# Performance work log

Measured on AMD Instinct MI355X. Metric: run time of the kernel, lower is better.

## Reference

```python
import jax, jax.numpy as jnp
import numpy as np

N_NODES = 50000
N_EDGES = 800000
H_DIM = 128
HIDDEN = 256


def _glorot(key, shape):
    fan_in, fan_out = shape[1], shape[0]
    lim = np.sqrt(6.0 / (fan_in + fan_out)).astype(np.float32)
    return jax.random.uniform(key, shape, jnp.float32, -lim, lim)


def setup_inputs() -> dict:
    key = jax.random.key(0)
    ks = jax.random.split(key, 12)
    h = jax.random.normal(ks[0], (N_NODES, H_DIM), jnp.float32)
    coord_diff = jax.random.normal(ks[1], (N_EDGES, 3), jnp.float32)
    row = jax.random.randint(ks[2], (N_EDGES,), 0, N_NODES, jnp.int64)
    col = jax.random.randint(ks[3], (N_EDGES,), 0, N_NODES, jnp.int64)
    # edge MLP: Linear(2*H+1 -> HIDDEN), SiLU, Linear(HIDDEN -> HIDDEN), SiLU
    We1 = _glorot(ks[4], (HIDDEN, 2 * H_DIM + 1))
    be1 = jnp.zeros((HIDDEN,), jnp.float32)
    We2 = _glorot(ks[5], (HIDDEN, HIDDEN))
    be2 = jnp.zeros((HIDDEN,), jnp.float32)
    # node MLP: Linear(HIDDEN + H -> HIDDEN), SiLU, Linear(HIDDEN -> H)
    Wn1 = _glorot(ks[6], (HIDDEN, HIDDEN + H_DIM))
    bn1 = jnp.zeros((HIDDEN,), jnp.float32)
    Wn2 = _glorot(ks[7], (H_DIM, HIDDEN))
    bn2 = jnp.zeros((H_DIM,), jnp.float32)
    return {"h": h, "coord_diff": coord_diff, "row": row, "col": col,
            "We1": We1, "be1": be1, "We2": We2, "be2": be2,
            "Wn1": Wn1, "bn1": bn1, "Wn2": Wn2, "bn2": bn2}


def reference(h, coord_diff, row, col, We1, be1, We2, be2, Wn1, bn1, Wn2, bn2):
    # radial: squared edge length, [E, 1]
    radial = jnp.sum(coord_diff ** 2, axis=1, keepdims=True)
    # edge model: gather endpoints, concat, 2-layer SiLU MLP
    e_in = jnp.concatenate([h[row], h[col], radial], axis=1)  # [E, 2H+1]
    m = jax.nn.silu(e_in @ We1.T + be1)                        # [E, HIDDEN]
    m = jax.nn.silu(m @ We2.T + be2)                           # [E, HIDDEN]
    # node model: scatter-add messages to source node `row`
    agg = jax.ops.segment_sum(m, row, num_segments=h.shape[0])  # [N, HIDDEN]
    n_in = jnp.concatenate([h, agg], axis=1)                    # [N, HIDDEN+H]
    out = jax.nn.silu(n_in @ Wn1.T + bn1) @ Wn2.T + bn2         # [N, H]
    return out
```

## Files before the change

kernel.cpp:

```cpp
#include <hip/hip_runtime.h>
#include <cstdint>
#include <cstddef>

#define E_EDGES 800000
#define N_NODES 50000
#define HDIM 128
#define HID 256
#define ME 64
#define NB 64
#define NTILES 196

typedef __attribute__((ext_vector_type(8))) short short8;
typedef __attribute__((ext_vector_type(4))) float f32x4;
typedef __attribute__((ext_vector_type(2))) float f32x2;
typedef __attribute__((ext_vector_type(4))) unsigned int u32x4;

__device__ __forceinline__ float silu(float y) {
    return y * __builtin_amdgcn_rcpf(1.0f + __expf(-y));
}

__device__ __forceinline__ f32x2 silu2(f32x2 y) {
    f32x2 nn = y * (-1.44269504f);
    f32x2 e;
    e.x = __builtin_amdgcn_exp2f(nn.x);
    e.y = __builtin_amdgcn_exp2f(nn.y);
    f32x2 den = e + 1.0f;
    f32x2 r;
    r.x = __builtin_amdgcn_rcpf(den.x);
    r.y = __builtin_amdgcn_rcpf(den.y);
    return y * r;
}

__device__ __forceinline__ f32x2 unpk(unsigned int d) {
    f32x2 r;
    r.x = __uint_as_float(d << 16);
    r.y = __uint_as_float(d & 0xFFFF0000u);
    return r;
}

__device__ __forceinline__ short f2bfn(float f) {
    __bf16 b = (__bf16)f;
    return __builtin_bit_cast(short, b);
}
__device__ __forceinline__ float bf2f(short s) {
    return __uint_as_float(((unsigned int)(unsigned short)s) << 16);
}

#define PREP_H    6250
#define PREP_AGG  (PREP_H + 12500)
#define PREP_HIST (PREP_AGG + 3125)
#define PREP_WAB  (PREP_HIST + 320)
#define PREP_WRF  (PREP_WAB + 1)
#define PREP_WE2  (PREP_WRF + 288)
#define PREP_WN1  (PREP_WE2 + 416)
#define PREP_WN2  (PREP_WN1 + 144)
__global__ void prep_kernel(const float* __restrict__ h, short* __restrict__ hbf,
                            float* __restrict__ agg,
                            const int* __restrict__ row, int* __restrict__ cnt,
                            const float* __restrict__ We1, const float* __restrict__ be1,
                            short* __restrict__ Wab, float* __restrict__ wrf,
                            const float* __restrict__ We2, const float* __restrict__ be2,
                            short* __restrict__ Wb2,
                            const float* __restrict__ Wn1, const float* __restrict__ bn1,
                            short* __restrict__ Wbn1,
                            const float* __restrict__ Wn2, const float* __restrict__ bn2,
                            short* __restrict__ Wbn2) {
    const int b = blockIdx.x, t = threadIdx.x;
    if (b < PREP_H) {
        int i = b * 256 + t;
        float4 v = ((const float4*)h)[i];
        short4 s;
        s.x = f2bfn(v.x); s.y = f2bfn(v.y); s.z = f2bfn(v.z); s.w = f2bfn(v.w);
        ((short4*)hbf)[i] = s;
    } else if (b < PREP_AGG) {
        int i = (b - PREP_H) * 256 + t;
        ((float4*)agg)[i] = make_float4(0.f, 0.f, 0.f, 0.f);
    } else if (b < PREP_HIST) {
        int e = (b - PREP_AGG) * 256 + t;
        if (e < E_EDGES) atomicAdd(&cnt[row[e]], 1);
    } else if (b < PREP_WAB) {
        int idx = (b - PREP_HIST) * 256 + t;
        int c = idx / 160, k = idx - c * 160;
        short v = 0;
        if (c < 256) {
            if (k < 128)       v = f2bfn(We1[c * 257 + k]);
            else if (k == 128) v = f2bfn(be1[c]);
        } else {
            if (k < 128)       v = f2bfn(We1[(c - 256) * 257 + 128 + k]);
        }
        Wab[idx] = v;
    } else if (b < PREP_WRF) {
        wrf[t] = We1[t * 257 + 256];
    } else if (b < PREP_WE2) {
        int idx = (b - PREP_WRF) * 256 + t;
        int c = idx / 288, k = idx - c * 288;
        short v = 0;
        if (k < 256)       v = f2bfn(We2[c * 256 + k]);
        else if (k == 256) v = f2bfn(be2[c]);
        Wb2[idx] = v;
    } else if (b < PREP_WN1) {
        int idx = (b - PREP_WE2) * 256 + t;
        int c = idx / 416, k = idx - c * 416;
        short v = 0;
        if (k < 384)       v = f2bfn(Wn1[c * 384 + k]);
        else if (k == 384) v = f2bfn(bn1[c]);
        Wbn1[idx] = v;
    } else {
        int idx = (b - PREP_WN1) * 256 + t;
        int c = idx / 288, k = idx - c * 288;
        short v = 0;
        if (k < 256)       v = f2bfn(Wn2[c * 256 + k]);
        else if (k == 256) v = f2bfn(bn2[c]);
        Wbn2[idx] = v;
    }
}

__global__ void scanA_kernel(const int* __restrict__ cnt, int* __restrict__ incl,
                             int* __restrict__ tsum) {
    const int b = blockIdx.x, t = threadIdx.x;
    const int i = b * 256 + t;
    const int lane = t & 63, wv = t >> 6;
    int v = (i < N_NODES) ? cnt[i] : 0;
    int s = v;
#pragma unroll
    for (int off = 1; off < 64; off <<= 1) {
        int u = __shfl_up(s, off, 64);
        if (lane >= off) s += u;
    }
    __shared__ int wsum[4];
    if (lane == 63) wsum[wv] = s;
    __syncthreads();
    int pre = 0;
#pragma unroll
    for (int j = 0; j < 3; ++j) if (wv > j) pre += wsum[j];
    s += pre;
    if (i < N_NODES) incl[i] = s;
    if (t == 255) tsum[b] = s;
}

__global__ void scanB_kernel(const int* __restrict__ tsum, int* __restrict__ toff) {
    const int t = threadIdx.x;
    const int lane = t & 63, wv = t >> 6;
    int v = (t < NTILES) ? tsum[t] : 0;
    int s = v;
#pragma unroll
    for (int off = 1; off < 64; off <<= 1) {
        int u = __shfl_up(s, off, 64);
        if (lane >= off) s += u;
    }
    __shared__ int wsum[4];
    if (lane == 63) wsum[wv] = s;
    __syncthreads();
    int pre = 0;
#pragma unroll
    for (int j = 0; j < 3; ++j) if (wv > j) pre += wsum[j];
    s += pre;
    if (t < NTILES) toff[t] = s - v;
}

__global__ void scanC_kernel(const int* __restrict__ cnt, int* __restrict__ cursor,
                             const int* __restrict__ toff) {
    const int b = blockIdx.x, t = threadIdx.x;
    const int i = b * 256 + t;
    if (i < N_NODES) {
        cursor[i] = cursor[i] - cnt[i] + toff[b];
    }
}

__global__ void fill_kernel(const int* __restrict__ row, int* __restrict__ cursor,
                            int* __restrict__ eidx) {
    int e = blockIdx.x * 256 + threadIdx.x;
    if (e < E_EDGES) {
        int pos = atomicAdd(&cursor[row[e]], 1);
        eidx[pos] = e;
    }
}

__global__ __launch_bounds__(256, 4) void hab_kernel(
    const short* __restrict__ hbf, const short* __restrict__ Wab,
    short* __restrict__ hab)
{
    __shared__ __align__(16) short pool[NB * 256];
    __shared__ __align__(16) short shTh[NB * 32];
    short* shH = pool;
    short* shO = pool;

    const int t = threadIdx.x;
    const int tile = blockIdx.x >> 1;
    const int half = blockIdx.x & 1;
    const int n0 = tile * NB;

    {
        const int n = t >> 2, q = t & 3;
        int gn = n0 + n;
        if (gn >= N_NODES) gn = N_NODES - 1;
        const short8* hp = (const short8*)(hbf + (size_t)gn * HDIM + q * 32);
#pragma unroll
        for (int c = 0; c < 4; ++c) {
            short8 v = hp[c];
            int chunk = q * 4 + c;
            *(short8*)&shH[n * 128 + ((chunk ^ (n & 7)) << 3)] = v;
        }
        short8 z = {0, 0, 0, 0, 0, 0, 0, 0};
        if (q == 0) z[0] = (short)0x3F80;
        *(short8*)&shTh[n * 32 + ((q ^ (n & 3)) << 3)] = z;
    }
    __syncthreads();

    const int l = t & 63, w = t >> 6;
    const int l15 = l & 15, lq = l >> 4;

    f32x4 acc[4][4];
#pragma unroll
    for (int i = 0; i < 4; ++i)
#pragma unroll
        for (int j = 0; j < 4; ++j) acc[i][j] = (f32x4){0.f, 0.f, 0.f, 0.f};

#pragma unroll
    for (int ks = 0; ks < 5; ++ks) {
        short8 a[4], b[4];
#pragma unroll
        for (int et = 0; et < 4; ++et) {
            int r = et * 16 + l15;
            if (ks < 4) {
                int chunk = ks * 4 + lq;
                a[et] = *(const short8*)&shH[r * 128 + ((chunk ^ (r & 7)) << 3)];
            } else {
                a[et] = *(const short8*)&shTh[r * 32 + ((lq ^ (r & 3)) << 3)];
            }
        }
#pragma unroll
        for (int ct = 0; ct < 4; ++ct) {
            int cc = half * 256 + w * 64 + ct * 16 + l15;
            b[ct] = *(const short8*)&Wab[cc * 160 + ks * 32 + lq * 8];
        }
#pragma unroll
        for (int et = 0; et < 4; ++et)
#pragma unroll
            for (int ct = 0; ct < 4; ++ct)
                acc[ct][et] = __builtin_amdgcn_mfma_f32_16x16x32_bf16(
                    b[ct], a[et], acc[ct][et], 0, 0, 0);
    }
    __syncthreads();

    {
#pragma unroll
        for (int ct = 0; ct < 4; ++ct) {
#pragma unroll
            for (int et = 0; et < 4; ++et) {
                int n = et * 16 + l15;
                int chb = w * 64 + ct * 16 + lq * 4;
                short4 s;
                s.x = f2bfn(acc[ct][et][0]);
                s.y = f2bfn(acc[ct][et][1]);
                s.z = f2bfn(acc[ct][et][2]);
                s.w = f2bfn(acc[ct][et][3]);
                int chunk = chb >> 3;
                *(short4*)&shO[n * 256 + ((chunk ^ (n & 7)) << 3) + (chb & 7)] = s;
            }
        }
    }
    __syncthreads();

    {
        const int n = t >> 2, q = t & 3;
        int gn = n0 + n;
        if (gn < N_NODES) {
            short* dst = hab + (size_t)gn * 512 + half * 256;
#pragma unroll
            for (int c = 0; c < 8; ++c) {
                int chunk = c * 4 + q;
                short8 v = *(const short8*)&shO[n * 256 + ((chunk ^ (n & 7)) << 3)];
                *(short8*)&dst[chunk * 8] = v;
            }
        }
    }
}

__global__ __launch_bounds__(256, 4) void edge_kernel(
    const short* __restrict__ hab, const float* __restrict__ coord,
    const int* __restrict__ row, const int* __restrict__ col,
    const int* __restrict__ eidx, const float* __restrict__ wrf,
    const short* __restrict__ Wb2, float* __restrict__ agg)
{
    __shared__ __align__(16) short shPool[ME * 256 + ME * 32];
    __shared__ int sr[ME];
    short* shA = shPool;
    short* shT = shPool + ME * 256;

    const int t = threadIdx.x;
    const int nwg = E_EDGES / ME;
    const int qq = nwg >> 3, rr = nwg & 7;
    const int xcd = blockIdx.x & 7, bi = blockIdx.x >> 3;
    const int wg = (xcd < rr ? xcd * (qq + 1) : rr * (qq + 1) + (xcd - rr) * qq) + bi;
    const int e0 = wg * ME;

    {
        const int e = t >> 2, q = t & 3;
        const int eo = eidx[e0 + e];
        const int rsrc = row[eo];
        const int csrc = col[eo];
        const short8* Ap = (const short8*)(hab + (size_t)rsrc * 512 + q * 64);
        const short8* Bp = (const short8*)(hab + (size_t)csrc * 512 + 256 + q * 64);
        short8 av[8], bv[8];
#pragma unroll
        for (int j = 0; j < 8; ++j) av[j] = Ap[j];
#pragma unroll
        for (int j = 0; j < 8; ++j) bv[j] = Bp[j];
        float cx = coord[3 * eo + 0];
        float cy = coord[3 * eo + 1];
        float cz = coord[3 * eo + 2];
        float radial = cx * cx + cy * cy + cz * cz;
        const f32x2* Wp2 = (const f32x2*)(wrf + q * 64);
#pragma unroll
        for (int j = 0; j < 8; ++j) {
            u32x4 ua = __builtin_bit_cast(u32x4, av[j]);
            u32x4 ub = __builtin_bit_cast(u32x4, bv[j]);
            short8 o;
#pragma unroll
            for (int u = 0; u < 4; ++u) {
                f32x2 af = unpk(ua[u]);
                f32x2 bf = unpk(ub[u]);
                f32x2 y = af + bf;
                y += radial * Wp2[4 * j + u];
                f32x2 s2 = silu2(y);
                o[2 * u]     = f2bfn(s2.x);
                o[2 * u + 1] = f2bfn(s2.y);
            }
            int chunk = q * 8 + j;
            *(short8*)&shA[e * 256 + ((chunk ^ (e & 7)) << 3)] = o;
        }
        short8 z = {0, 0, 0, 0, 0, 0, 0, 0};
        if (q == 0) {
            z[0] = (short)0x3F80;
            sr[e] = rsrc;
        }
        *(short8*)&shT[e * 32 + ((q ^ (e & 3)) << 3)] = z;
    }
    __syncthreads();

    const int l = t & 63, w = t >> 6;
    const int l15 = l & 15, lq = l >> 4;

    f32x4 acc[4][4];
#pragma unroll
    for (int i = 0; i < 4; ++i)
#pragma unroll
        for (int j = 0; j < 4; ++j) acc[i][j] = (f32x4){0.f, 0.f, 0.f, 0.f};
#pragma unroll
    for (int ks = 0; ks < 8; ++ks) {
        short8 a[4], b[4];
#pragma unroll
        for (int et = 0; et < 4; ++et) {
            int r = et * 16 + l15;
            int chunk = ks * 4 + lq;
            a[et] = *(const short8*)&shA[r * 256 + ((chunk ^ (r & 7)) << 3)];
        }
#pragma unroll
        for (int ct = 0; ct < 4; ++ct) {
            int cc = w * 64 + ct * 16 + l15;
            b[ct] = *(const short8*)&Wb2[cc * 288 + ks * 32 + lq * 8];
        }
        __builtin_amdgcn_s_setprio(1);
#pragma unroll
        for (int et = 0; et < 4; ++et)
#pragma unroll
            for (int ct = 0; ct < 4; ++ct)
                acc[et][ct] = __builtin_amdgcn_mfma_f32_16x16x32_bf16(
                    a[et], b[ct], acc[et][ct], 0, 0, 0);
        __builtin_amdgcn_s_setprio(0);
    }
    {
        short8 a[4], b[4];
#pragma unroll
        for (int et = 0; et < 4; ++et) {
            int r = et * 16 + l15;
            a[et] = *(const short8*)&shT[r * 32 + ((lq ^ (r & 3)) << 3)];
        }
#pragma unroll
        for (int ct = 0; ct < 4; ++ct) {
            int cc = w * 64 + ct * 16 + l15;
            b[ct] = *(const short8*)&Wb2[cc * 288 + 256 + lq * 8];
        }
        __builtin_amdgcn_s_setprio(1);
#pragma unroll
        for (int et = 0; et < 4; ++et)
#pragma unroll
            for (int ct = 0; ct < 4; ++ct)
                acc[et][ct] = __builtin_amdgcn_mfma_f32_16x16x32_bf16(
                    a[et], b[ct], acc[et][ct], 0, 0, 0);
        __builtin_amdgcn_s_setprio(0);
    }
    __syncthreads();

    {
#pragma unroll
        for (int ct = 0; ct < 4; ++ct) {
#pragma unroll
            for (int et = 0; et < 4; ++et) {
                int kc = w * 64 + ct * 16 + l15;
                int er0 = et * 16 + lq * 4;
                f32x2 p0 = {acc[et][ct][0], acc[et][ct][1]};
                f32x2 p1 = {acc[et][ct][2], acc[et][ct][3]};
                f32x2 s0 = silu2(p0);
                f32x2 s1 = silu2(p1);
                short4 s;
                s.x = f2bfn(s0.x);
                s.y = f2bfn(s0.y);
                s.z = f2bfn(s1.x);
                s.w = f2bfn(s1.y);
                *(short4*)&shPool[kc * 68 + er0] = s;
            }
        }
    }
    __syncthreads();

    {
        const int cc = t;
        const short* myrow = &shPool[cc * 68];
        float accum = 0.f;
        int cur = __builtin_amdgcn_readfirstlane(sr[0]);
        bool headSeg = true;
        for (int eb = 0; eb < ME; eb += 4) {
            short4 v4 = *(const short4*)&myrow[eb];
            short vj[4] = {v4.x, v4.y, v4.z, v4.w};
#pragma unroll
            for (int j = 0; j < 4; ++j) {
                float v = bf2f(vj[j]);
                int r = __builtin_amdgcn_readfirstlane(sr[eb + j]);
                if (r != cur) {
                    if (headSeg) {
                        atomicAdd(&agg[(size_t)cur * HID + cc], accum);
                        headSeg = false;
                    } else {
                        agg[(size_t)cur * HID + cc] = accum;
                    }
                    accum = v;
                    cur = r;
                } else {
                    accum += v;
                }
            }
        }
        atomicAdd(&agg[(size_t)cur * HID + cc], accum);
    }
}

__global__ __launch_bounds__(256, 3) void node_kernel(
    const short* __restrict__ hbf, const float* __restrict__ agg,
    const short* __restrict__ Wbn1, const short* __restrict__ Wbn2,
    float* __restrict__ out)
{
    __shared__ __align__(16) short pool[NB * 384];
    __shared__ __align__(16) short shTn[NB * 32];
    short* shH  = pool;
    short* shAg = pool + NB * 128;
    short* shM  = pool;

    const int t  = threadIdx.x;
    const int n0 = blockIdx.x * NB;

    {
        const int n = t >> 2, q = t & 3;
        int gn = n0 + n;
        if (gn >= N_NODES) gn = N_NODES - 1;
        const short8* hp = (const short8*)(hbf + (size_t)gn * HDIM + q * 32);
#pragma unroll
        for (int c = 0; c < 4; ++c) {
            short8 v = hp[c];
            int chunk = q * 4 + c;
            int sw = chunk ^ (n & 7);
            *(short8*)&shH[n * 128 + sw * 8] = v;
        }
        const float4* ap = (const float4*)(agg + (size_t)gn * HID + q * 64);
#pragma unroll
        for (int i = 0; i < 8; ++i) {
            float4 u0 = ap[2 * i], u1 = ap[2 * i + 1];
            short8 s;
            s[0] = f2bfn(u0.x); s[1] = f2bfn(u0.y); s[2] = f2bfn(u0.z); s[3] = f2bfn(u0.w);
            s[4] = f2bfn(u1.x); s[5] = f2bfn(u1.y); s[6] = f2bfn(u1.z); s[7] = f2bfn(u1.w);
            int chunk = q * 8 + i;
            int sw2 = chunk ^ (n & 7);
            *(short8*)&shAg[n * 256 + sw2 * 8] = s;
        }
        short8 z = {0, 0, 0, 0, 0, 0, 0, 0};
        if (q == 0) z[0] = (short)0x3F80;
        *(short8*)&shTn[n * 32 + ((q ^ (n & 3)) << 3)] = z;
    }
    __syncthreads();

    const int l = t & 63, w = t >> 6;
    const int l15 = l & 15, lq = l >> 4;

    f32x4 acc[4][4];
#pragma unroll
    for (int i = 0; i < 4; ++i)
#pragma unroll
        for (int j = 0; j < 4; ++j) acc[i][j] = (f32x4){0.f, 0.f, 0.f, 0.f};
#pragma unroll
    for (int ks = 0; ks < 12; ++ks) {
        short8 a[4], b[4];
#pragma unroll
        for (int et = 0; et < 4; ++et) {
            int r = et * 16 + l15;
            if (ks < 4) {
                int chunk = ks * 4 + lq;
                a[et] = *(const short8*)&shH[r * 128 + ((chunk ^ (r & 7)) << 3)];
            } else {
                int chunk = (ks - 4) * 4 + lq;
                a[et] = *(const short8*)&shAg[r * 256 + ((chunk ^ (r & 7)) << 3)];
            }
        }
#pragma unroll
        for (int ct = 0; ct < 4; ++ct) {
            int cc = w * 64 + ct * 16 + l15;
            b[ct] = *(const short8*)&Wbn1[cc * 416 + ks * 32 + lq * 8];
        }
#pragma unroll
        for (int et = 0; et < 4; ++et)
#pragma unroll
            for (int ct = 0; ct < 4; ++ct)
                acc[et][ct] = __builtin_amdgcn_mfma_f32_16x16x32_bf16(
                    a[et], b[ct], acc[et][ct], 0, 0, 0);
    }
    {
        short8 a[4], b[4];
#pragma unroll
        for (int et = 0; et < 4; ++et) {
            int r = et * 16 + l15;
            a[et] = *(const short8*)&shTn[r * 32 + ((lq ^ (r & 3)) << 3)];
        }
#pragma unroll
        for (int ct = 0; ct < 4; ++ct) {
            int cc = w * 64 + ct * 16 + l15;
            b[ct] = *(const short8*)&Wbn1[cc * 416 + 384 + lq * 8];
        }
#pragma unroll
        for (int et = 0; et < 4; ++et)
#pragma unroll
            for (int ct = 0; ct < 4; ++ct)
                acc[et][ct] = __builtin_amdgcn_mfma_f32_16x16x32_bf16(
                    a[et], b[ct], acc[et][ct], 0, 0, 0);
    }
    __syncthreads();

    {
#pragma unroll
        for (int et = 0; et < 4; ++et) {
#pragma unroll
            for (int rp = 0; rp < 2; ++rp) {
                int er0 = et * 16 + lq * 4 + rp * 2;
#pragma unroll
                for (int ct = 0; ct < 4; ++ct) {
                    int kc = w * 64 + ct * 16 + l15;
                    float y0 = silu(acc[et][ct][rp * 2]);
                    float y1 = silu(acc[et][ct][rp * 2 + 1]);
                    int khi = kc >> 3, klo = kc & 7;
                    shM[er0 * 256 + ((khi ^ (er0 & 7)) << 3) + klo] = f2bfn(y0);
                    shM[(er0 + 1) * 256 + ((khi ^ ((er0 + 1) & 7)) << 3) + klo] = f2bfn(y1);
                }
            }
        }
    }
    __syncthreads();

    f32x4 acc2[4][2];
#pragma unroll
    for (int i = 0; i < 4; ++i)
#pragma unroll
        for (int j = 0; j < 2; ++j) acc2[i][j] = (f32x4){0.f, 0.f, 0.f, 0.f};
#pragma unroll
    for (int ks = 0; ks < 8; ++ks) {
        short8 a[4], b2[2];
#pragma unroll
        for (int et = 0; et < 4; ++et) {
            int r = et * 16 + l15;
            int chunk = ks * 4 + lq;
            a[et] = *(const short8*)&shM[r * 256 + ((chunk ^ (r & 7)) << 3)];
        }
#pragma unroll
        for (int ct = 0; ct < 2; ++ct) {
            int cc = w * 32 + ct * 16 + l15;
            b2[ct] = *(const short8*)&Wbn2[cc * 288 + ks * 32 + lq * 8];
        }
#pragma unroll
        for (int et = 0; et < 4; ++et)
#pragma unroll
            for (int ct = 0; ct < 2; ++ct)
                acc2[et][ct] = __builtin_amdgcn_mfma_f32_16x16x32_bf16(
                    a[et], b2[ct], acc2[et][ct], 0, 0, 0);
    }
    {
        short8 a[4], b2[2];
#pragma unroll
        for (int et = 0; et < 4; ++et) {
            int r = et * 16 + l15;
            a[et] = *(const short8*)&shTn[r * 32 + ((lq ^ (r & 3)) << 3)];
        }
#pragma unroll
        for (int ct = 0; ct < 2; ++ct) {
            int cc = w * 32 + ct * 16 + l15;
            b2[ct] = *(const short8*)&Wbn2[cc * 288 + 256 + lq * 8];
        }
#pragma unroll
        for (int et = 0; et < 4; ++et)
#pragma unroll
            for (int ct = 0; ct < 2; ++ct)
                acc2[et][ct] = __builtin_amdgcn_mfma_f32_16x16x32_bf16(
                    a[et], b2[ct], acc2[et][ct], 0, 0, 0);
    }

#pragma unroll
    for (int et = 0; et < 4; ++et) {
#pragma unroll
        for (int ct = 0; ct < 2; ++ct) {
            int cc = w * 32 + ct * 16 + l15;
#pragma unroll
            for (int r4 = 0; r4 < 4; ++r4) {
                int gn = n0 + et * 16 + lq * 4 + r4;
                if (gn < N_NODES)
                    out[(size_t)gn * HDIM + cc] = acc2[et][ct][r4];
            }
        }
    }
}

extern "C" void kernel_launch(void* const* d_in, const int* in_sizes, int n_in,
                              void* d_out, int out_size, void* d_ws, size_t ws_size,
                              hipStream_t stream) {
    const float* h   = (const float*)d_in[0];
    const float* cd  = (const float*)d_in[1];
    const int*   row = (const int*)d_in[2];
    const int*   col = (const int*)d_in[3];
    const float* We1 = (const float*)d_in[4];
    const float* be1 = (const float*)d_in[5];
    const float* We2 = (const float*)d_in[6];
    const float* be2 = (const float*)d_in[7];
    const float* Wn1 = (const float*)d_in[8];
    const float* bn1 = (const float*)d_in[9];
    const float* Wn2 = (const float*)d_in[10];
    const float* bn2 = (const float*)d_in[11];
    float* out = (float*)d_out;

    short* Wab  = (short*)d_ws;
    short* Wb2  = Wab + 512 * 160;
    short* Wbn1 = Wb2 + 256 * 288;
    short* Wbn2 = Wbn1 + 256 * 416;
    float* wrf  = (float*)(Wbn2 + 128 * 288);
    short* hbf  = (short*)(wrf + 256);
    short* hab  = hbf + (size_t)N_NODES * HDIM;
    float* agg  = (float*)(hab + (size_t)N_NODES * 512);
    int*   cnt    = (int*)(agg + (size_t)N_NODES * HID);
    int*   cursor = cnt + N_NODES;
    int*   eidx   = cursor + N_NODES;
    int*   tsum   = eidx + E_EDGES;
    int*   toff   = tsum + 256;

    hipMemsetAsync(cnt, 0, N_NODES * sizeof(int), stream);

    prep_kernel<<<PREP_WN2, 256, 0, stream>>>(h, hbf, agg, row, cnt,
                                              We1, be1, Wab, wrf,
                                              We2, be2, Wb2,
                                              Wn1, bn1, Wbn1, Wn2, bn2, Wbn2);

    hab_kernel<<<((N_NODES + NB - 1) / NB) * 2, 256, 0, stream>>>(hbf, Wab, hab);

    scanA_kernel<<<NTILES, 256, 0, stream>>>(cnt, cursor, tsum);
    scanB_kernel<<<1, 256, 0, stream>>>(tsum, toff);
    scanC_kernel<<<NTILES, 256, 0, stream>>>(cnt, cursor, toff);
    fill_kernel<<<(E_EDGES + 255) / 256, 256, 0, stream>>>(row, cursor, eidx);

    edge_kernel<<<E_EDGES / ME, 256, 0, stream>>>(hab, cd, row, col, eidx, wrf,
                                                  Wb2, agg);
    node_kernel<<<(N_NODES + NB - 1) / NB, 256, 0, stream>>>(hbf, agg, Wbn1, Wbn2, out);
}
```

Before: 474.4 us.

## Sort edges by column bucket then row to improve gather locality

Edges are now counting-sorted by a composite key of (col bucket of 6250 nodes, row) instead of by row alone. Each edge tile then gathers col-endpoint features from a narrow node range, which is meant to improve L2 reuse of the hab gathers. The cost is an 8x larger histogram and scan (400k keys across 1563 tiles, with a multi-element-per-thread top-level scan). Because one row's edges are now split across buckets, segment flushes can no longer use plain stores and every flush becomes an atomicAdd, adding atomic traffic on agg.

```diff
diff --git a/kernel.cpp b/kernel.cpp
--- a/kernel.cpp
+++ b/kernel.cpp
@@ -8,7 +8,9 @@
 #define HID 256
 #define ME 64
 #define NB 64
-#define NTILES 196
+#define NBUK_DIV 6250
+#define NKEYS 400000
+#define NT2 1563
 
 typedef __attribute__((ext_vector_type(8))) short short8;
 typedef __attribute__((ext_vector_type(4))) float f32x4;
@@ -56,7 +58,8 @@
 #define PREP_WN2  (PREP_WN1 + 144)
 __global__ void prep_kernel(const float* __restrict__ h, short* __restrict__ hbf,
                             float* __restrict__ agg,
-                            const int* __restrict__ row, int* __restrict__ cnt,
+                            const int* __restrict__ row, const int* __restrict__ col,
+                            int* __restrict__ cnt,
                             const float* __restrict__ We1, const float* __restrict__ be1,
                             short* __restrict__ Wab, float* __restrict__ wrf,
                             const float* __restrict__ We2, const float* __restrict__ be2,
@@ -77,7 +80,10 @@
         ((float4*)agg)[i] = make_float4(0.f, 0.f, 0.f, 0.f);
     } else if (b < PREP_HIST) {
         int e = (b - PREP_AGG) * 256 + t;
-        if (e < E_EDGES) atomicAdd(&cnt[row[e]], 1);
+        if (e < E_EDGES) {
+            int key = (col[e] / NBUK_DIV) * N_NODES + row[e];
+            atomicAdd(&cnt[key], 1);
+        }
     } else if (b < PREP_WAB) {
         int idx = (b - PREP_HIST) * 256 + t;
         int c = idx / 160, k = idx - c * 160;
@@ -120,7 +126,7 @@
     const int b = blockIdx.x, t = threadIdx.x;
     const int i = b * 256 + t;
     const int lane = t & 63, wv = t >> 6;
-    int v = (i < N_NODES) ? cnt[i] : 0;
+    int v = (i < NKEYS) ? cnt[i] : 0;
     int s = v;
 #pragma unroll
     for (int off = 1; off < 64; off <<= 1) {
@@ -134,15 +140,25 @@
 #pragma unroll
     for (int j = 0; j < 3; ++j) if (wv > j) pre += wsum[j];
     s += pre;
-    if (i < N_NODES) incl[i] = s;
+    if (i < NKEYS) incl[i] = s;
     if (t == 255) tsum[b] = s;
 }
 
 __global__ void scanB_kernel(const int* __restrict__ tsum, int* __restrict__ toff) {
     const int t = threadIdx.x;
     const int lane = t & 63, wv = t >> 6;
-    int v = (t < NTILES) ? tsum[t] : 0;
-    int s = v;
+    int vex[7];
+    int run = 0;
+    const int base = t * 7;
+#pragma unroll
+    for (int k = 0; k < 7; ++k) {
+        int idx = base + k;
+        int x = (idx < NT2) ? tsum[idx] : 0;
+        vex[k] = run;
+        run += x;
+    }
+    int tot = run;
+    int s = tot;
 #pragma unroll
     for (int off = 1; off < 64; off <<= 1) {
         int u = __shfl_up(s, off, 64);
@@ -155,23 +171,29 @@
 #pragma unroll
     for (int j = 0; j < 3; ++j) if (wv > j) pre += wsum[j];
     s += pre;
-    if (t < NTILES) toff[t] = s - v;
+    int excl = s - tot;
+#pragma unroll
+    for (int k = 0; k < 7; ++k) {
+        int idx = base + k;
+        if (idx < NT2) toff[idx] = excl + vex[k];
+    }
 }
 
 __global__ void scanC_kernel(const int* __restrict__ cnt, int* __restrict__ cursor,
                              const int* __restrict__ toff) {
     const int b = blockIdx.x, t = threadIdx.x;
     const int i = b * 256 + t;
-    if (i < N_NODES) {
+    if (i < NKEYS) {
         cursor[i] = cursor[i] - cnt[i] + toff[b];
     }
 }
 
-__global__ void fill_kernel(const int* __restrict__ row, int* __restrict__ cursor,
-                            int* __restrict__ eidx) {
+__global__ void fill_kernel(const int* __restrict__ row, const int* __restrict__ col,
+                            int* __restrict__ cursor, int* __restrict__ eidx) {
     int e = blockIdx.x * 256 + threadIdx.x;
     if (e < E_EDGES) {
-        int pos = atomicAdd(&cursor[row[e]], 1);
+        int key = (col[e] / NBUK_DIV) * N_NODES + row[e];
+        int pos = atomicAdd(&cursor[key], 1);
         eidx[pos] = e;
     }
 }
@@ -420,7 +442,6 @@
         const short* myrow = &shPool[cc * 68];
         float accum = 0.f;
         int cur = __builtin_amdgcn_readfirstlane(sr[0]);
-        bool headSeg = true;
         for (int eb = 0; eb < ME; eb += 4) {
             short4 v4 = *(const short4*)&myrow[eb];
             short vj[4] = {v4.x, v4.y, v4.z, v4.w};
@@ -429,12 +450,7 @@
                 float v = bf2f(vj[j]);
                 int r = __builtin_amdgcn_readfirstlane(sr[eb + j]);
                 if (r != cur) {
-                    if (headSeg) {
-                        atomicAdd(&agg[(size_t)cur * HID + cc], accum);
-                        headSeg = false;
-                    } else {
-                        agg[(size_t)cur * HID + cc] = accum;
-                    }
+                    atomicAdd(&agg[(size_t)cur * HID + cc], accum);
                     accum = v;
                     cur = r;
                 } else {
@@ -651,24 +667,24 @@
     short* hab  = hbf + (size_t)N_NODES * HDIM;
     float* agg  = (float*)(hab + (size_t)N_NODES * 512);
     int*   cnt    = (int*)(agg + (size_t)N_NODES * HID);
-    int*   cursor = cnt + N_NODES;
-    int*   eidx   = cursor + N_NODES;
+    int*   cursor = cnt + NKEYS;
+    int*   eidx   = cursor + NKEYS;
     int*   tsum   = eidx + E_EDGES;
-    int*   toff   = tsum + 256;
-
-    hipMemsetAsync(cnt, 0, N_NODES * sizeof(int), stream);
-
-    prep_kernel<<<PREP_WN2, 256, 0, stream>>>(h, hbf, agg, row, cnt,
+    int*   toff   = tsum + 2048;
+
+    hipMemsetAsync(cnt, 0, NKEYS * sizeof(int), stream);
+
+    prep_kernel<<<PREP_WN2, 256, 0, stream>>>(h, hbf, agg, row, col, cnt,
                                               We1, be1, Wab, wrf,
                                               We2, be2, Wb2,
                                               Wn1, bn1, Wbn1, Wn2, bn2, Wbn2);
 
     hab_kernel<<<((N_NODES + NB - 1) / NB) * 2, 256, 0, stream>>>(hbf, Wab, hab);
 
-    scanA_kernel<<<NTILES, 256, 0, stream>>>(cnt, cursor, tsum);
+    scanA_kernel<<<NT2, 256, 0, stream>>>(cnt, cursor, tsum);
     scanB_kernel<<<1, 256, 0, stream>>>(tsum, toff);
-    scanC_kernel<<<NTILES, 256, 0, stream>>>(cnt, cursor, toff);
-    fill_kernel<<<(E_EDGES + 255) / 256, 256, 0, stream>>>(row, cursor, eidx);
+    scanC_kernel<<<NT2, 256, 0, stream>>>(cnt, cursor, toff);
+    fill_kernel<<<(E_EDGES + 255) / 256, 256, 0, stream>>>(row, col, cursor, eidx);
 
     edge_kernel<<<E_EDGES / ME, 256, 0, stream>>>(hab, cd, row, col, eidx, wrf,
                                                   Wb2, agg);
```

New measurement: 544.9 us. +14.8%, slower.
